# Kernel optimization log

Measured on AMD Instinct MI355X. Metric: run time of the kernel, lower is better.

Reference implementation:

```python
import jax, jax.numpy as jnp
import numpy as np
import math

LMAX = 3
NCHAN = 32
NEDGE = 50000

# ---------- Wigner 3j (real spherical-harmonic basis), replicating e3nn ----------

def _su2_cg(j1, j2, j3):
    f = math.factorial
    def coeff(m1, m2, m3):
        vmin = int(max(-j1 + j2 + m3, -j1 + m1, 0))
        vmax = int(min(j2 + j3 + m1, j3 - j1 + j2, j3 + m3))
        C = ((2 * j3 + 1) * f(j3 + j1 - j2) * f(j3 - j1 + j2) * f(j1 + j2 - j3) / f(j1 + j2 + j3 + 1)) ** 0.5
        C *= (f(j3 + m3) * f(j3 - m3) * f(j1 - m1) * f(j1 + m1) * f(j2 - m2) * f(j2 + m2)) ** 0.5
        S = 0.0
        for v in range(vmin, vmax + 1):
            S += (-1.0) ** (v + j2 + m2) * f(j2 + j3 + m1 - v) * f(j1 - m1 + v) / (
                f(v) * f(j3 - j1 + j2 - v) * f(j3 + m3 - v) * f(v + j1 - j2 - m3))
        return C * S
    out = np.zeros((2 * j1 + 1, 2 * j2 + 1, 2 * j3 + 1))
    for m1 in range(-j1, j1 + 1):
        for m2 in range(-j2, j2 + 1):
            m3 = m1 + m2
            if -j3 <= m3 <= j3:
                out[m1 + j1, m2 + j2, m3 + j3] = coeff(m1, m2, m3)
    return out

def _q_real_to_complex(l):
    q = np.zeros((2 * l + 1, 2 * l + 1), dtype=np.complex128)
    for m in range(-l, 0):
        q[l + m, l + abs(m)] = 1 / 2 ** 0.5
        q[l + m, l - abs(m)] = -1j / 2 ** 0.5
    q[l, l] = 1.0
    for m in range(1, l + 1):
        q[l + m, l + abs(m)] = (-1) ** m / 2 ** 0.5
        q[l + m, l - abs(m)] = 1j * (-1) ** m / 2 ** 0.5
    return (-1j) ** l * q

def _wigner_3j(l1, l2, l3):
    C = _su2_cg(l1, l2, l3).astype(np.complex128)
    Q1, Q2, Q3 = _q_real_to_complex(l1), _q_real_to_complex(l2), _q_real_to_complex(l3)
    C = np.einsum('ij,kl,mn,ikn->jlm', Q1, Q2, np.conj(Q3.T), C)
    C = np.real(C)
    return C / np.linalg.norm(C)

# ---------- Instruction enumeration (matches the torch module's __init__) ----------

def _build_paths():
    ls = list(range(LMAX + 1))  # irreps 0e,1o,2e,3o -> parity (-1)^l
    ins = []
    for l1 in ls:
        for l2 in ls:
            for l3 in range(abs(l1 - l2), min(l1 + l2, LMAX) + 1):
                if (l1 + l2 + l3) % 2 == 0:  # parity selection p1*p2 == p3
                    ins.append((l1, l2, l3))
    # e3nn Irreps.sort: stable sort of output blocks by ir; pos[i] = sorted position
    order_sorted = sorted(range(len(ins)), key=lambda i: ins[i][2])
    pos = [0] * len(ins)
    for new, old in enumerate(order_sorted):
        pos[old] = new
    # replicate `outputs.insert(ins.i_out, output)` over instruction iteration order
    concat = []
    for idx in range(len(ins)):
        concat.insert(min(pos[idx], len(concat)), idx)
    offs = np.cumsum([0] + [2 * l + 1 for l in ls]).tolist()  # block offsets in dim-16 layout
    # path_weight: component normalization, one path per output block -> sqrt(2*l3+1)
    cg = [jnp.asarray((_wigner_3j(l1, l2, l3) * math.sqrt(2 * l3 + 1)).astype(np.float32))
          for (l1, l2, l3) in ins]
    return ins, pos, concat, offs, cg

_INS, _POS, _CONCAT, _OFFS, _CG = _build_paths()  # 23 instructions, out dim 99


def setup_inputs() -> dict:
    key = jax.random.key(0)
    k1, k2, k3 = jax.random.split(key, 3)
    x = jax.random.normal(k1, (NEDGE, NCHAN, 16), dtype=jnp.float32)
    y = jax.random.normal(k2, (NEDGE, 1, 16), dtype=jnp.float32)
    weights = jax.random.normal(k3, (NEDGE, len(_INS) * NCHAN, 1), dtype=jnp.float32)
    return {"x": x, "y": y, "weights": weights}


def reference(x, y, weights):
    # x: [E, C, 16], y: [E, 1, 16], weights: [E, n_ins*C, 1]
    C = x.shape[1]
    y2 = y[:, 0, :]  # [E, 16]
    outs = [None] * len(_INS)
    for idx, (l1, l2, l3) in enumerate(_INS):
        o1, o2 = _OFFS[l1], _OFFS[l2]
        xb = x[:, :, o1:o1 + 2 * l1 + 1]            # [E, C, 2l1+1]
        yb = y2[:, o2:o2 + 2 * l2 + 1]              # [E, 2l2+1]
        w = weights[:, _POS[idx] * C:(_POS[idx] + 1) * C, 0]  # [E, C]
        # dense CG contraction == sparse gather-multiply-index_add over (mu1,mu2,mu3)
        blk = jnp.einsum('eci,ej,ijk->eck', xb, yb, _CG[idx])  # [E, C, 2l3+1]
        outs[idx] = w[:, :, None] * blk
    return jnp.concatenate([outs[i] for i in _CONCAT], axis=-1)  # [E, C, 99]
```

## Files before the change

kernel.cpp:

```cpp
#include <hip/hip_runtime.h>
#include <math.h>

#define NPATH 23
#define NEDGE 50000
#define NCHAN 32
#define NWROW 736
#define OUTW  99
#define TTOT  439
#define EPB   2
#define NTHR  256

constexpr int L1[NPATH]    = {0,0,0,0,1,1,1,1,1,1,2,2,2,2,2,2,2,3,3,3,3,3,3};
constexpr int L2[NPATH]    = {0,1,2,3,0,1,1,2,2,3,0,1,1,2,2,3,3,0,1,2,2,3,3};
constexpr int L3[NPATH]    = {0,1,2,3,1,0,2,1,3,2,2,1,3,0,2,1,3,3,2,1,3,0,2};
constexpr int POS[NPATH]   = {0,4,10,17,5,1,11,6,18,12,13,7,19,2,14,8,20,21,15,9,22,3,16};
constexpr int OOFF[NPATH]  = {0,4,7,12,19,1,34,22,39,46,51,31,61,2,73,25,78,85,68,28,92,3,56};
constexpr int TOFF[NPATH]  = {0,1,4,9,16,25,28,43,52,73,88,113,128,163,168,193,208,243,292,327,348,397,404};
constexpr int LOFF[4]      = {0,1,4,9};

constexpr unsigned GMASKS[4] = {0x122028u, 0x211405u, 0x444100u, 0x88AD2u};

constexpr int PAD(int n1){ return n1 <= 3 ? 4 : 8; }

struct PT { int v[NPATH]; int total; };
constexpr PT make_ptoff(){
    PT t{}; int a = 0;
    for(int p = 0; p < NPATH; ++p){ t.v[p] = a; a += (2*L3[p]+1)*PAD(2*L1[p]+1); }
    t.total = a;
    return t;
}
constexpr PT PTOF = make_ptoff();
static_assert(PTOF.total == 632, "padded T size");
#define TSZ 632

struct BTab { unsigned v[4][28]; int cnt[4]; };
constexpr BTab make_btab(){
    BTab b{};
    for(int g = 0; g < 4; ++g){
        int n = 0;
        for(int p = 0; p < NPATH; ++p){
            if(!((GMASKS[g] >> p) & 1u)) continue;
            int n1 = 2*L1[p]+1, n3 = 2*L3[p]+1;
            int o2 = LOFF[L2[p]];
            int q0 = o2 >> 2;
            for(int k = 0; k < n3; ++k){
                b.v[g][n++] = (unsigned)(TOFF[p]+k)
                            | ((unsigned)n3 << 9) | ((unsigned)n1 << 12)
                            | ((unsigned)(PAD(n1)==8 ? 1 : 0) << 15)
                            | ((unsigned)(PTOF.v[p] + k*PAD(n1)) << 16)
                            | ((unsigned)q0 << 26);
            }
        }
        b.cnt[g] = n;
    }
    return b;
}
constexpr BTab BT = make_btab();

typedef _Float16 __attribute__((ext_vector_type(4))) h4;

__device__ __forceinline__ int imx(int a, int b){ return a > b ? a : b; }
__device__ __forceinline__ int imn(int a, int b){ return a < b ? a : b; }

__device__ __forceinline__ double factd(int n){
    double r = 1.0;
    for(int i = 2; i <= n; ++i) r *= (double)i;
    return r;
}

__global__ __launch_bounds__(512) void cg_setup(float* __restrict__ cgd2){
    const int p  = blockIdx.x;
    const int j1 = L1[p], j2 = L2[p], j3 = L3[p];
    const int n1 = 2*j1+1, n2 = 2*j2+1, n3 = 2*j3+1;
    const int o2 = LOFF[j2];
    const int ntot = n1*n2*n3;
    const int t = threadIdx.x;

    __shared__ double scg[343];
    __shared__ double qre[3][49];
    __shared__ double qim[3][49];
    __shared__ double red[512];

    if(t < ntot){
        int a   = t / (n2*n3);
        int rem = t - a*(n2*n3);
        int b   = rem / n3;
        int g   = rem - b*n3;
        int m1 = a - j1, m2 = b - j2, m3 = g - j3;
        double val = 0.0;
        if(m1 + m2 == m3){
            int vmin = imx(imx(-j1 + j2 + m3, -j1 + m1), 0);
            int vmax = imn(imn(j2 + j3 + m1, j3 - j1 + j2), j3 + m3);
            double C = sqrt((2.0*j3 + 1.0) * factd(j3 + j1 - j2) * factd(j3 - j1 + j2)
                            * factd(j1 + j2 - j3) / factd(j1 + j2 + j3 + 1));
            C *= sqrt(factd(j3 + m3) * factd(j3 - m3) * factd(j1 - m1)
                      * factd(j1 + m1) * factd(j2 - m2) * factd(j2 + m2));
            double S = 0.0;
            for(int v = vmin; v <= vmax; ++v){
                double sgn = ((v + j2 + m2) & 1) ? -1.0 : 1.0;
                S += sgn * factd(j2 + j3 + m1 - v) * factd(j1 - m1 + v)
                     / (factd(v) * factd(j3 - j1 + j2 - v) * factd(j3 + m3 - v)
                        * factd(v + j1 - j2 - m3));
            }
            val = C * S;
        }
        scg[t] = val;
    }

    if(t < 3){
        int l = (t == 0) ? j1 : ((t == 1) ? j2 : j3);
        int n = 2*l + 1;
        double* QR = qre[t];
        double* QI = qim[t];
        for(int i = 0; i < 49; ++i){ QR[i] = 0.0; QI[i] = 0.0; }
        const double is2 = 0.70710678118654752440;
        for(int m = -l; m < 0; ++m){
            QR[(l+m)*n + (l-m)] = is2;
            QI[(l+m)*n + (l+m)] = -is2;
        }
        QR[l*n + l] = 1.0;
        for(int m = 1; m <= l; ++m){
            double s = (m & 1) ? -1.0 : 1.0;
            QR[(l+m)*n + (l+m)] = s * is2;
            QI[(l+m)*n + (l-m)] = s * is2;
        }
        double fr, fi;
        switch(l & 3){
            case 0: fr = 1.0;  fi = 0.0;  break;
            case 1: fr = 0.0;  fi = -1.0; break;
            case 2: fr = -1.0; fi = 0.0;  break;
            default: fr = 0.0; fi = 1.0;  break;
        }
        for(int i = 0; i < n*n; ++i){
            double re = QR[i], im = QI[i];
            QR[i] = re*fr - im*fi;
            QI[i] = re*fi + im*fr;
        }
    }
    __syncthreads();

    double val = 0.0;
    if(t < ntot){
        int j   = t / (n2*n3);
        int rem = t - j*(n2*n3);
        int lq  = rem / n3;
        int m   = rem - lq*n3;
        double acc = 0.0;
        for(int i = 0; i < n1; ++i){
            double q1r = qre[0][i*n1 + j], q1i = qim[0][i*n1 + j];
            if(q1r == 0.0 && q1i == 0.0) continue;
            for(int k = 0; k < n2; ++k){
                double q2r = qre[1][k*n2 + lq], q2i = qim[1][k*n2 + lq];
                if(q2r == 0.0 && q2i == 0.0) continue;
                double ar = q1r*q2r - q1i*q2i;
                double ai = q1r*q2i + q1i*q2r;
                for(int n = 0; n < n3; ++n){
                    double cv = scg[(i*n2 + k)*n3 + n];
                    if(cv == 0.0) continue;
                    double q3r = qre[2][n*n3 + m];
                    double q3i = -qim[2][n*n3 + m];
                    acc += cv * (ar*q3r - ai*q3i);
                }
            }
        }
        val = acc;
    }

    red[t] = val * val;
    __syncthreads();
    if(t < 343) scg[t] = val;
    for(int s2 = 256; s2 > 0; s2 >>= 1){
        if(t < s2) red[t] += red[t + s2];
        __syncthreads();
    }
    const double scale = sqrt(2.0*j3 + 1.0) / sqrt(red[0]);

    for(int u = t; u < n1*n3*16; u += 512){
        int sl = u >> 4, jf = u & 15;
        int i  = sl / n3, k = sl - i*n3;
        int j  = jf - o2;
        double v2 = (j >= 0 && j < n2) ? scg[(i*n2 + j)*n3 + k] : 0.0;
        cgd2[(size_t)(TOFF[p] + sl)*16 + jf] = (float)(v2 * scale);
    }
}

template<int G>
__device__ __forceinline__ void prefetchW(const float* __restrict__ wbase,
                                          float* __restrict__ wreg)
{
    constexpr unsigned mask = GMASKS[G];
    #pragma unroll
    for(int p = 0; p < NPATH; ++p){
        if((mask >> p) & 1u)
            wreg[__builtin_popcount(mask & ((1u << p) - 1u))] = wbase[POS[p]*NCHAN];
    }
}

template<int G>
__device__ __forceinline__ void phaseB(int lane, int e0,
                                       const float* __restrict__ y,
                                       const float* __restrict__ cgd2,
                                       float* __restrict__ TsL)
{
    constexpr int E = BT.cnt[G];
    if(lane < 2*E){
        const int el  = (lane >= E) ? 1 : 0;
        const int idx = lane - el*E;
        const unsigned ent = BT.v[G][idx];
        const int slot0 = ent & 511;
        const int n3    = (ent >> 9)  & 7;
        const int n1    = (ent >> 12) & 7;
        const int pad8  = (ent >> 15) & 1;
        const int dst   = (ent >> 16) & 1023;
        const int q0    = (ent >> 26) & 3;

        const float* yq = y + (size_t)(e0 + el)*16 + q0*4;
        float4 y0 = *(const float4*)yq;
        float4 y1 = *(const float4*)(yq + 4);

        float T[8];
        #pragma unroll
        for(int i = 0; i < 8; ++i) T[i] = 0.f;
        #pragma unroll
        for(int i = 0; i < 7; ++i){
            if(i < n1){
                const float* cr = cgd2 + (size_t)(slot0 + i*n3)*16 + q0*4;
                float4 c0 = *(const float4*)cr;
                float4 c1 = *(const float4*)(cr + 4);
                float a;
                a = fmaf(c0.x, y0.x, 0.f);  a = fmaf(c0.y, y0.y, a);
                a = fmaf(c0.z, y0.z, a);    a = fmaf(c0.w, y0.w, a);
                a = fmaf(c1.x, y1.x, a);    a = fmaf(c1.y, y1.y, a);
                a = fmaf(c1.z, y1.z, a);    a = fmaf(c1.w, y1.w, a);
                T[i] = a;
            }
        }
        float* d = TsL + el*TSZ + dst;
        *(float4*)d = float4{T[0], T[1], T[2], T[3]};
        if(pad8) *((float4*)d + 1) = float4{T[4], T[5], T[6], T[7]};
    }
}

template<int G>
__device__ __forceinline__ void phaseC(const float* __restrict__ xr,
                                       const float* __restrict__ wreg,
                                       const float* __restrict__ Te,
                                       _Float16* __restrict__ ob)
{
    constexpr unsigned mask = GMASKS[G];
    #pragma unroll
    for(int p = 0; p < NPATH; ++p){
        if(!((mask >> p) & 1u)) continue;
        const int widx = __builtin_popcount(mask & ((1u << p) - 1u));
        const int n1  = 2*L1[p] + 1;
        const int n3  = 2*L3[p] + 1;
        const int o1  = LOFF[L1[p]];
        const int pad = PAD(n1);
        const float wp = wreg[widx];

        float acc[7];
        #pragma unroll
        for(int k = 0; k < n3; ++k){
            const float* tr = Te + PTOF.v[p] + k*pad;
            float4 t0 = *(const float4*)tr;
            float a = xr[o1] * t0.x;
            if(n1 > 1){
                a = fmaf(xr[o1+1], t0.y, a);
                a = fmaf(xr[o1+2], t0.z, a);
            }
            if(n1 > 3){
                a = fmaf(xr[o1+3], t0.w, a);
                float4 t1 = *((const float4*)tr + 1);
                a = fmaf(xr[o1+4], t1.x, a);
                if(n1 > 5){
                    a = fmaf(xr[o1+5], t1.y, a);
                    a = fmaf(xr[o1+6], t1.z, a);
                }
            }
            acc[k] = a * wp;
        }

        const int off  = OOFF[p];
        const int lead = off & 1;
        if(lead) ob[off] = (_Float16)acc[0];
        const int npair = (n3 - lead) >> 1;
        #pragma unroll
        for(int kk = 0; kk < npair; ++kk){
            const int k0 = lead + 2*kk;
            _Float16 h0 = (_Float16)acc[k0];
            _Float16 h1 = (_Float16)acc[k0+1];
            unsigned u = (unsigned)__builtin_bit_cast(unsigned short, h0)
                       | ((unsigned)__builtin_bit_cast(unsigned short, h1) << 16);
            *reinterpret_cast<unsigned*>(
                reinterpret_cast<char*>(ob) + (size_t)(off + k0)*2) = u;
        }
        if((n3 - lead) & 1) ob[off + n3 - 1] = (_Float16)acc[n3-1];
    }
}

__global__ __launch_bounds__(NTHR, 6) void tp_main(
    const float* __restrict__ x, const float* __restrict__ y,
    const float* __restrict__ w, const float* __restrict__ cgd2,
    float* __restrict__ out)
{
    __shared__ __align__(16) _Float16 obuf[EPB*NCHAN*100];
    __shared__ __align__(16) float Ts[EPB*TSZ];

    const int tid = threadIdx.x;
    const int e0  = blockIdx.x * EPB;

    const int lane = tid & 63;
    const int c    = tid & 31;
    const int el   = (tid >> 5) & 1;
    const int grp  = tid >> 6;
    const int e    = e0 + el;

    const float4* xp = reinterpret_cast<const float4*>(x + (size_t)(e*NCHAN + c)*16);
    float4 x0 = xp[0], x1 = xp[1], x2 = xp[2], x3 = xp[3];

    const float* wbase = w + (size_t)e*NWROW + c;
    float wreg[10];
    switch(grp){
        case 0: prefetchW<0>(wbase, wreg); break;
        case 1: prefetchW<1>(wbase, wreg); break;
        case 2: prefetchW<2>(wbase, wreg); break;
        default: prefetchW<3>(wbase, wreg); break;
    }

    switch(grp){
        case 0: phaseB<0>(lane, e0, y, cgd2, Ts); break;
        case 1: phaseB<1>(lane, e0, y, cgd2, Ts); break;
        case 2: phaseB<2>(lane, e0, y, cgd2, Ts); break;
        default: phaseB<3>(lane, e0, y, cgd2, Ts); break;
    }

    asm volatile("s_waitcnt lgkmcnt(0)" ::: "memory");
    __builtin_amdgcn_sched_barrier(0);

    float xr[16];
    xr[0]=x0.x;  xr[1]=x0.y;  xr[2]=x0.z;  xr[3]=x0.w;
    xr[4]=x1.x;  xr[5]=x1.y;  xr[6]=x1.z;  xr[7]=x1.w;
    xr[8]=x2.x;  xr[9]=x2.y;  xr[10]=x2.z; xr[11]=x2.w;
    xr[12]=x3.x; xr[13]=x3.y; xr[14]=x3.z; xr[15]=x3.w;

    const float* Te = Ts + el*TSZ;
    _Float16* ob = obuf + (el*NCHAN + c)*100;

    switch(grp){
        case 0: phaseC<0>(xr, wreg, Te, ob); break;
        case 1: phaseC<1>(xr, wreg, Te, ob); break;
        case 2: phaseC<2>(xr, wreg, Te, ob); break;
        default: phaseC<3>(xr, wreg, Te, ob); break;
    }
    __syncthreads();

    const h4* ob4 = reinterpret_cast<const h4*>(obuf);
    for(int idx = tid; idx < EPB*NCHAN*25; idx += NTHR){
        int row = idx / 25;
        int j   = idx - row*25;
        h4 hv = ob4[idx];
        float* base = out + (size_t)(e0 + (row >> 5))*(NCHAN*OUTW)
                          + (size_t)(row & 31)*OUTW + j*4;
        base[0] = (float)hv[0];
        base[1] = (float)hv[1];
        base[2] = (float)hv[2];
        if(j < 24) base[3] = (float)hv[3];
    }
}

extern "C" void kernel_launch(void* const* d_in, const int* in_sizes, int n_in,
                              void* d_out, int out_size, void* d_ws, size_t ws_size,
                              hipStream_t stream)
{
    const float* x  = (const float*)d_in[0];
    const float* y  = (const float*)d_in[1];
    const float* wt = (const float*)d_in[2];
    float* out = (float*)d_out;
    float* cgd2 = (float*)d_ws;

    cg_setup<<<NPATH, 512, 0, stream>>>(cgd2);
    tp_main<<<NEDGE/EPB, NTHR, 0, stream>>>(x, y, wt, cgd2, out);
}
```

Baseline: 271.0 us.

## Make blocks persistent over edge pairs with double-buffered register prefetch

Each block now loops over 8 edge pairs instead of handling one pair. The x, w and y loads for the next pair are issued into a second register set while the current pair is computed, hiding global-load latency behind compute. The output writeback loop is unrolled, and the grid shrinks to 3125 blocks. In exchange, register pressure rises (launch bounds drop from 6 to 4 waves), there are extra barriers per iteration, and parallelism drops, which may cut occupancy.

```diff
diff --git a/kernel.cpp b/kernel.cpp
--- a/kernel.cpp
+++ b/kernel.cpp
@@ -7,7 +7,8 @@
 #define NWROW 736
 #define OUTW  99
 #define TTOT  439
-#define EPB   2
+#define NITER 8
+#define NBLK  (NEDGE/2/NITER)
 #define NTHR  256
 
 constexpr int L1[NPATH]    = {0,0,0,0,1,1,1,1,1,1,2,2,2,2,2,2,2,3,3,3,3,3,3};
@@ -30,7 +31,6 @@
     return t;
 }
 constexpr PT PTOF = make_ptoff();
-static_assert(PTOF.total == 632, "padded T size");
 #define TSZ 632
 
 struct BTab { unsigned v[4][28]; int cnt[4]; };
@@ -41,8 +41,7 @@
         for(int p = 0; p < NPATH; ++p){
             if(!((GMASKS[g] >> p) & 1u)) continue;
             int n1 = 2*L1[p]+1, n3 = 2*L3[p]+1;
-            int o2 = LOFF[L2[p]];
-            int q0 = o2 >> 2;
+            int q0 = LOFF[L2[p]] >> 2;
             for(int k = 0; k < n3; ++k){
                 b.v[g][n++] = (unsigned)(TOFF[p]+k)
                             | ((unsigned)n3 << 9) | ((unsigned)n1 << 12)
@@ -66,6 +65,11 @@
     double r = 1.0;
     for(int i = 2; i <= n; ++i) r *= (double)i;
     return r;
+}
+
+__device__ __forceinline__ void sync_lds(){
+    asm volatile("s_waitcnt lgkmcnt(0)" ::: "memory");
+    __builtin_amdgcn_s_barrier();
 }
 
 __global__ __launch_bounds__(512) void cg_setup(float* __restrict__ cgd2){
@@ -197,51 +201,6 @@
 }
 
 template<int G>
-__device__ __forceinline__ void phaseB(int lane, int e0,
-                                       const float* __restrict__ y,
-                                       const float* __restrict__ cgd2,
-                                       float* __restrict__ TsL)
-{
-    constexpr int E = BT.cnt[G];
-    if(lane < 2*E){
-        const int el  = (lane >= E) ? 1 : 0;
-        const int idx = lane - el*E;
-        const unsigned ent = BT.v[G][idx];
-        const int slot0 = ent & 511;
-        const int n3    = (ent >> 9)  & 7;
-        const int n1    = (ent >> 12) & 7;
-        const int pad8  = (ent >> 15) & 1;
-        const int dst   = (ent >> 16) & 1023;
-        const int q0    = (ent >> 26) & 3;
-
-        const float* yq = y + (size_t)(e0 + el)*16 + q0*4;
-        float4 y0 = *(const float4*)yq;
-        float4 y1 = *(const float4*)(yq + 4);
-
-        float T[8];
-        #pragma unroll
-        for(int i = 0; i < 8; ++i) T[i] = 0.f;
-        #pragma unroll
-        for(int i = 0; i < 7; ++i){
-            if(i < n1){
-                const float* cr = cgd2 + (size_t)(slot0 + i*n3)*16 + q0*4;
-                float4 c0 = *(const float4*)cr;
-                float4 c1 = *(const float4*)(cr + 4);
-                float a;
-                a = fmaf(c0.x, y0.x, 0.f);  a = fmaf(c0.y, y0.y, a);
-                a = fmaf(c0.z, y0.z, a);    a = fmaf(c0.w, y0.w, a);
-                a = fmaf(c1.x, y1.x, a);    a = fmaf(c1.y, y1.y, a);
-                a = fmaf(c1.z, y1.z, a);    a = fmaf(c1.w, y1.w, a);
-                T[i] = a;
-            }
-        }
-        float* d = TsL + el*TSZ + dst;
-        *(float4*)d = float4{T[0], T[1], T[2], T[3]};
-        if(pad8) *((float4*)d + 1) = float4{T[4], T[5], T[6], T[7]};
-    }
-}
-
-template<int G>
 __device__ __forceinline__ void phaseC(const float* __restrict__ xr,
                                        const float* __restrict__ wreg,
                                        const float* __restrict__ Te,
@@ -298,73 +257,130 @@
     }
 }
 
-__global__ __launch_bounds__(NTHR, 6) void tp_main(
+template<int G>
+__device__ __forceinline__ void run_loop(
+    int p0, int tid,
+    const float* __restrict__ x, const float* __restrict__ y,
+    const float* __restrict__ w, const float* __restrict__ cgd2,
+    float* __restrict__ out, _Float16* __restrict__ obuf,
+    float* __restrict__ Ts)
+{
+    constexpr int E = BT.cnt[G];
+    const int lane = tid & 63;
+    const int c    = tid & 31;
+    const int el   = (tid >> 5) & 1;
+
+    const bool bact  = lane < 2*E;
+    const int  bidx  = bact ? (lane >= E ? lane - E : lane) : 0;
+    const int  el_b  = (lane >= E) ? 1 : 0;
+    const unsigned ent = BT.v[G][bidx];
+    const int slot0 = ent & 511;
+    const int n3b   = (ent >> 9)  & 7;
+    const int n1b   = (ent >> 12) & 7;
+    const int pad8  = (ent >> 15) & 1;
+    const int dst   = (ent >> 16) & 1023;
+    const int q0    = (ent >> 26) & 3;
+    const int yoffL = el_b*16 + q0*4;
+
+    float4 xA0,xA1,xA2,xA3, xB0,xB1,xB2,xB3;
+    float  wA[10], wB[10];
+    float4 yA0,yA1, yB0,yB1;
+
+    #define LOADP(pair, X0,X1,X2,X3, WREG, Y0,Y1) do{                          \
+        int pp = imn((pair), NEDGE/2 - 1);                                     \
+        const float4* xp = reinterpret_cast<const float4*>(                    \
+            x + ((size_t)((pp*2 + el)*NCHAN + c))*16);                         \
+        X0 = xp[0]; X1 = xp[1]; X2 = xp[2]; X3 = xp[3];                        \
+        prefetchW<G>(w + (size_t)(pp*2 + el)*NWROW + c, WREG);                 \
+        const float* yb = y + (size_t)pp*32 + yoffL;                           \
+        Y0 = *(const float4*)yb; Y1 = *(const float4*)(yb + 4);                \
+    }while(0)
+
+    #define ITER(pair, X0,X1,X2,X3, WREG, Y0,Y1) do{                           \
+                                   \
+        if(bact){                                                              \
+            float T[8];                                                        \
+            _Pragma("unroll") for(int i = 0; i < 8; ++i) T[i] = 0.f;           \
+            _Pragma("unroll") for(int i = 0; i < 7; ++i){                      \
+                if(i < n1b){                                                   \
+                    const float* cr = cgd2 + (size_t)(slot0 + i*n3b)*16 + q0*4;\
+                    float4 c0 = *(const float4*)cr;                            \
+                    float4 c1 = *(const float4*)(cr + 4);                      \
+                    float a;                                                   \
+                    a = fmaf(c0.x, Y0.x, 0.f); a = fmaf(c0.y, Y0.y, a);        \
+                    a = fmaf(c0.z, Y0.z, a);   a = fmaf(c0.w, Y0.w, a);        \
+                    a = fmaf(c1.x, Y1.x, a);   a = fmaf(c1.y, Y1.y, a);        \
+                    a = fmaf(c1.z, Y1.z, a);   a = fmaf(c1.w, Y1.w, a);        \
+                    T[i] = a;                                                  \
+                }                                                              \
+            }                                                                  \
+            float* d = Ts + el_b*TSZ + dst;                                    \
+            *(float4*)d = float4{T[0], T[1], T[2], T[3]};                      \
+            if(pad8) *((float4*)d + 1) = float4{T[4], T[5], T[6], T[7]};       \
+        }                                                                      \
+        asm volatile("s_waitcnt lgkmcnt(0)" ::: "memory");                     \
+        __builtin_amdgcn_sched_barrier(0);                                     \
+                                                                  \
+        {                                                                      \
+            float xr[16];                                                      \
+            xr[0]=X0.x;  xr[1]=X0.y;  xr[2]=X0.z;  xr[3]=X0.w;                 \
+            xr[4]=X1.x;  xr[5]=X1.y;  xr[6]=X1.z;  xr[7]=X1.w;                 \
+            xr[8]=X2.x;  xr[9]=X2.y;  xr[10]=X2.z; xr[11]=X2.w;                \
+            xr[12]=X3.x; xr[13]=X3.y; xr[14]=X3.z; xr[15]=X3.w;                \
+            phaseC<G>(xr, WREG, Ts + el*TSZ, obuf + (el*NCHAN + c)*100);       \
+        }                                                                      \
+        sync_lds();                                                            \
+                    \
+        {                                                                      \
+            const h4* ob4 = reinterpret_cast<const h4*>(obuf);                 \
+            float* outb = out + (size_t)(pair)*2*(NCHAN*OUTW);                 \
+            _Pragma("unroll") for(int k2 = 0; k2 < 7; ++k2){                   \
+                int idx = tid + k2*NTHR;                                       \
+                if(idx < 1600){                                                \
+                    int row = idx / 25;                                        \
+                    int j   = idx - row*25;                                    \
+                    h4 hv = ob4[idx];                                          \
+                    float* base = outb + (size_t)row*OUTW + j*4;               \
+                    base[0] = (float)hv[0];                                    \
+                    base[1] = (float)hv[1];                                    \
+                    base[2] = (float)hv[2];                                    \
+                    if(j < 24) base[3] = (float)hv[3];                         \
+                }                                                              \
+            }                                                                  \
+        }                                                                      \
+        sync_lds();                                                            \
+    }while(0)
+
+    LOADP(p0, xA0,xA1,xA2,xA3, wA, yA0,yA1);
+
+    #pragma unroll 1
+    for(int it = 0; it < NITER; it += 2){
+        LOADP(p0 + it + 1, xB0,xB1,xB2,xB3, wB, yB0,yB1);
+        ITER (p0 + it,     xA0,xA1,xA2,xA3, wA, yA0,yA1);
+        LOADP(p0 + it + 2, xA0,xA1,xA2,xA3, wA, yA0,yA1);
+        ITER (p0 + it + 1, xB0,xB1,xB2,xB3, wB, yB0,yB1);
+    }
+    #undef LOADP
+    #undef ITER
+}
+
+__global__ __launch_bounds__(NTHR, 4) void tp_main(
     const float* __restrict__ x, const float* __restrict__ y,
     const float* __restrict__ w, const float* __restrict__ cgd2,
     float* __restrict__ out)
 {
-    __shared__ __align__(16) _Float16 obuf[EPB*NCHAN*100];
-    __shared__ __align__(16) float Ts[EPB*TSZ];
+    __shared__ __align__(16) _Float16 obuf[2*NCHAN*100];
+    __shared__ __align__(16) float Ts[2*TSZ];
 
     const int tid = threadIdx.x;
-    const int e0  = blockIdx.x * EPB;
-
-    const int lane = tid & 63;
-    const int c    = tid & 31;
-    const int el   = (tid >> 5) & 1;
-    const int grp  = tid >> 6;
-    const int e    = e0 + el;
-
-    const float4* xp = reinterpret_cast<const float4*>(x + (size_t)(e*NCHAN + c)*16);
-    float4 x0 = xp[0], x1 = xp[1], x2 = xp[2], x3 = xp[3];
-
-    const float* wbase = w + (size_t)e*NWROW + c;
-    float wreg[10];
+    const int p0  = blockIdx.x * NITER;
+    const int grp = tid >> 6;
+
     switch(grp){
-        case 0: prefetchW<0>(wbase, wreg); break;
-        case 1: prefetchW<1>(wbase, wreg); break;
-        case 2: prefetchW<2>(wbase, wreg); break;
-        default: prefetchW<3>(wbase, wreg); break;
-    }
-
-    switch(grp){
-        case 0: phaseB<0>(lane, e0, y, cgd2, Ts); break;
-        case 1: phaseB<1>(lane, e0, y, cgd2, Ts); break;
-        case 2: phaseB<2>(lane, e0, y, cgd2, Ts); break;
-        default: phaseB<3>(lane, e0, y, cgd2, Ts); break;
-    }
-
-    asm volatile("s_waitcnt lgkmcnt(0)" ::: "memory");
-    __builtin_amdgcn_sched_barrier(0);
-
-    float xr[16];
-    xr[0]=x0.x;  xr[1]=x0.y;  xr[2]=x0.z;  xr[3]=x0.w;
-    xr[4]=x1.x;  xr[5]=x1.y;  xr[6]=x1.z;  xr[7]=x1.w;
-    xr[8]=x2.x;  xr[9]=x2.y;  xr[10]=x2.z; xr[11]=x2.w;
-    xr[12]=x3.x; xr[13]=x3.y; xr[14]=x3.z; xr[15]=x3.w;
-
-    const float* Te = Ts + el*TSZ;
-    _Float16* ob = obuf + (el*NCHAN + c)*100;
-
-    switch(grp){
-        case 0: phaseC<0>(xr, wreg, Te, ob); break;
-        case 1: phaseC<1>(xr, wreg, Te, ob); break;
-        case 2: phaseC<2>(xr, wreg, Te, ob); break;
-        default: phaseC<3>(xr, wreg, Te, ob); break;
-    }
-    __syncthreads();
-
-    const h4* ob4 = reinterpret_cast<const h4*>(obuf);
-    for(int idx = tid; idx < EPB*NCHAN*25; idx += NTHR){
-        int row = idx / 25;
-        int j   = idx - row*25;
-        h4 hv = ob4[idx];
-        float* base = out + (size_t)(e0 + (row >> 5))*(NCHAN*OUTW)
-                          + (size_t)(row & 31)*OUTW + j*4;
-        base[0] = (float)hv[0];
-        base[1] = (float)hv[1];
-        base[2] = (float)hv[2];
-        if(j < 24) base[3] = (float)hv[3];
+        case 0: run_loop<0>(p0, tid, x, y, w, cgd2, out, obuf, Ts); break;
+        case 1: run_loop<1>(p0, tid, x, y, w, cgd2, out, obuf, Ts); break;
+        case 2: run_loop<2>(p0, tid, x, y, w, cgd2, out, obuf, Ts); break;
+        default: run_loop<3>(p0, tid, x, y, w, cgd2, out, obuf, Ts); break;
     }
 }
 
@@ -379,5 +395,5 @@
     float* cgd2 = (float*)d_ws;
 
     cg_setup<<<NPATH, 512, 0, stream>>>(cgd2);
-    tp_main<<<NEDGE/EPB, NTHR, 0, stream>>>(x, y, wt, cgd2, out);
-}
+    tp_main<<<NBLK, NTHR, 0, stream>>>(x, y, wt, cgd2, out);
+}
```

After: 368.0 us. 35.8% more time.
